# Kernel tuning notes

Hardware: AMD Instinct MI355X
Metric: run time of the kernel (lower is better)

The kernel has to match this reference:

```python
import math
import jax, jax.numpy as jnp
from jax import lax
import numpy as np

# Dimensions (see shape_source)
B, CIN, COUT, H, W = 4, 256, 256, 128, 128
STYLE_DIM = 512
K = 3            # modulated-conv kernel
N_TAPS = 12      # FIR taps
UP, DOWN = 2, 2
UP_PAD, DOWN_PAD = 6, 5   # symmetric pads for up/down FIR stages
SLOPE = 0.2
CLAMP = 256.0
EPS = 1e-8


def _kaiser_lowpass(n_taps, cutoff, band_half, sr):
    # exact port of kaiser_window/lowpass_filter (1-D, use_jinc=False)
    df = 2.0 * band_half / (sr / 2.0)
    atten = 2.285 * (n_taps - 1) * math.pi * df + 7.95
    if atten > 50:
        beta = 0.1102 * (atten - 8.7)
    elif atten >= 21:
        beta = 0.5842 * (atten - 21) ** 0.4 + 0.07886 * (atten - 21)
    else:
        beta = 0.0
    ind = np.arange(n_taps) - (n_taps - 1) / 2.0
    window = np.i0(beta * np.sqrt(1 - (2 * ind / (n_taps - 1)) ** 2)) / np.i0(beta)
    f = 2 * cutoff / sr * np.sinc(2 * cutoff / sr * ind) * window
    return f.astype(np.float32)


def setup_inputs() -> dict:
    key = jax.random.key(0)
    k0, k1, k2, k3 = jax.random.split(key, 4)
    inputs = {
        "input": jax.random.normal(k0, (B, CIN, H, W), jnp.float32),
        "style": jax.random.normal(k1, (B, STYLE_DIM), jnp.float32),
        "weight": jax.random.normal(k2, (COUT, CIN, K, K), jnp.float32),
        "mod_weight": jax.random.normal(k3, (CIN, STYLE_DIM), jnp.float32),
        "mod_bias": jnp.ones((CIN,), jnp.float32),     # EqualLinear bias_init=1
        "bias": jnp.zeros((COUT,), jnp.float32),
        "up_filter": jnp.asarray(_kaiser_lowpass(N_TAPS, cutoff=H / 2, band_half=H / 2, sr=2 * H)),
        "down_filter": jnp.asarray(_kaiser_lowpass(N_TAPS, cutoff=H / 2, band_half=H / 2, sr=2 * H)),
    }
    return inputs


def _upfirdn2d_sep(x, f, up, down, pad):
    # separable depthwise FIR with zero-stuffed upsampling (lhs_dilation)
    c = x.shape[1]
    t = f.shape[0]
    fv = jnp.tile(f.reshape(1, 1, t, 1), (c, 1, 1, 1))
    x = lax.conv_general_dilated(x, fv, window_strides=(down, 1),
                                 padding=((pad, pad), (0, 0)), lhs_dilation=(up, 1),
                                 feature_group_count=c,
                                 dimension_numbers=("NCHW", "OIHW", "NCHW"))
    fh = jnp.tile(f.reshape(1, 1, 1, t), (c, 1, 1, 1))
    x = lax.conv_general_dilated(x, fh, window_strides=(1, down),
                                 padding=((0, 0), (pad, pad)), lhs_dilation=(1, up),
                                 feature_group_count=c,
                                 dimension_numbers=("NCHW", "OIHW", "NCHW"))
    return x


def reference(input, style, weight, mod_weight, mod_bias, bias, up_filter, down_filter):
    b, cin, h, w = input.shape
    # EqualLinear modulation: scale = 1/sqrt(style_dim), lr_mul=1, bias_init=1
    s = style @ mod_weight.T * (1.0 / math.sqrt(STYLE_DIM)) + mod_bias          # [B,Cin]
    # ModulatedConv2d (eval mode: input_gain = rsqrt(ema_var=1) = 1)
    w_mod = weight[None] * s[:, None, :, None, None]                            # [B,Cout,Cin,k,k]
    demod = lax.rsqrt(jnp.sum(w_mod * w_mod, axis=(2, 3, 4)) + EPS)             # [B,Cout]
    w_mod = (w_mod * demod[:, :, None, None, None]).reshape(b * COUT, cin, K, K)
    x = input.reshape(1, b * cin, h, w)
    out = lax.conv_general_dilated(x, w_mod, (1, 1),
                                   ((K - 1, K - 1), (K - 1, K - 1)),
                                   feature_group_count=b,
                                   dimension_numbers=("NCHW", "OIHW", "NCHW"))
    out = out.reshape(b, COUT, out.shape[2], out.shape[3])                      # [B,Cout,130,130]
    # filtered_lrelu: bias -> FIR up x2 (gain up^2 = up per separable pass)
    out = out + bias[None, :, None, None]
    out = _upfirdn2d_sep(out, up_filter * UP, UP, 1, UP_PAD)                    # [B,Cout,260,260]
    out = jnp.where(out >= 0, out, SLOPE * out) * math.sqrt(2.0)                # lrelu, gain sqrt(2)
    out = jnp.clip(out, -CLAMP, CLAMP)
    out = _upfirdn2d_sep(out, down_filter, 1, DOWN, DOWN_PAD)                   # [B,Cout,130,130]
    return out
```

## Files before the change

### kernel.cpp

```cpp
#include <hip/hip_runtime.h>
#include <hip/hip_bf16.h>
#include <math.h>

#define B_    4
#define CIN_  256
#define COUT_ 256
#define H_    128
#define W_    128
#define HW_   16384
#define SD_   512
#define HO_   130
#define HU_   260
#define NT_   12

typedef unsigned short ushort_t;
typedef __attribute__((ext_vector_type(8))) short short8;
typedef __attribute__((ext_vector_type(4))) float f32x4;

__device__ inline ushort_t f2bf_(float v) {
  union { float f; unsigned u; } x; x.f = v;
  unsigned r = x.u + 0x7fffu + ((x.u >> 16) & 1u);
  return (ushort_t)(r >> 16);
}
__device__ inline void gll16(const ushort_t* g, ushort_t* l) {
  __builtin_amdgcn_global_load_lds(
      (const __attribute__((address_space(1))) unsigned int*)g,
      (__attribute__((address_space(3))) unsigned int*)l, 16, 0, 0);
}

__global__ __launch_bounds__(256) void k_mod(const float* __restrict__ style,
                                             const float* __restrict__ mw,
                                             const float* __restrict__ mb,
                                             float* __restrict__ s) {
  int wid  = (blockIdx.x * blockDim.x + threadIdx.x) >> 6;
  int lane = threadIdx.x & 63;
  int b = wid >> 8, ci = wid & 255;
  const float* st = style + b * SD_;
  const float* w  = mw + ci * SD_;
  float acc = 0.f;
  for (int k = lane; k < SD_; k += 64) acc += st[k] * w[k];
  for (int off = 32; off; off >>= 1) acc += __shfl_down(acc, off);
  if (lane == 0) s[wid] = acc * 0.044194173824159216f + mb[ci];
}

__global__ __launch_bounds__(256) void k_demod(const float* __restrict__ weight,
                                               const float* __restrict__ s,
                                               float* __restrict__ demod) {
  int wid  = (blockIdx.x * blockDim.x + threadIdx.x) >> 6;
  int lane = threadIdx.x & 63;
  int b = wid >> 8, co = wid & 255;
  const float* wrow = weight + co * CIN_ * 9;
  const float* sb   = s + b * CIN_;
  float acc = 0.f;
  for (int e = lane; e < CIN_ * 9; e += 64) {
    float p = wrow[e] * sb[e / 9];
    acc += p * p;
  }
  for (int off = 32; off; off >>= 1) acc += __shfl_down(acc, off);
  if (lane == 0) demod[wid] = rsqrtf(acc + 1e-8f);
}

__global__ __launch_bounds__(256) void k_prep_w(const float* __restrict__ W,
                                                ushort_t* __restrict__ Wth) {
  int idx = blockIdx.x * 256 + threadIdx.x;
  if (idx >= 589824) return;
  int j  = idx & 7;
  int co = (idx >> 3) & 127;
  int kc = (idx >> 10) & 3;
  int kb = (idx >> 12) & 7;
  int cb = (idx >> 15) & 1;
  int t  = idx >> 16;
  int ci  = kb * 32 + kc * 8 + j;
  int cog = cb * 128 + co;
  Wth[idx] = f2bf_(W[(cog * CIN_ + ci) * 9 + t]);
}

__global__ __launch_bounds__(256) void k_prep_x(const float* __restrict__ input,
                                                const float* __restrict__ s,
                                                ushort_t* __restrict__ Xt,
                                                float* __restrict__ zp) {
  int b = blockIdx.z, cb = blockIdx.y, px0 = blockIdx.x * 64;
  int tid = threadIdx.x;
  __shared__ float T[64 * 131];
  __shared__ float sSh[128];
  if (tid < 128) sSh[tid] = s[b * 256 + cb * 128 + tid];
  if (blockIdx.x == 0 && blockIdx.y == 0 && blockIdx.z == 0 && tid < 4)
    zp[tid] = 0.f;
  __syncthreads();
  const float* inb = input + (size_t)(b * 256 + cb * 128) * HW_ + px0;
#pragma unroll
  for (int r2 = 0; r2 < 32; ++r2) {
    int idx = r2 * 256 + tid;
    int ci = idx >> 6, p = idx & 63;
    T[p * 131 + ci] = inb[(size_t)ci * HW_ + p] * sSh[ci];
  }
  __syncthreads();
  ushort_t* xb = Xt + (size_t)b * HW_ * 256 + cb * 128;
#pragma unroll
  for (int r2 = 0; r2 < 16; ++r2) {
    int u = r2 * 256 + tid;
    int cp = u & 63, p = u >> 6;
    float v0 = T[p * 131 + 2 * cp], v1 = T[p * 131 + 2 * cp + 1];
    unsigned pk = (unsigned)f2bf_(v0) | ((unsigned)f2bf_(v1) << 16);
    *(unsigned*)(xb + ((size_t)(px0 + p)) * 256 + cp * 2) = pk;
  }
}

#define XCELLS 864
#define XROUNDS 4
#define XBUFU  1024

__global__ __launch_bounds__(256, 3) void k_conv_mfma(
    const ushort_t* __restrict__ Xt, const ushort_t* __restrict__ Wth,
    const float* __restrict__ demod, const float* __restrict__ bias,
    const ushort_t* __restrict__ zpg, float* __restrict__ out1) {
  const int tid = threadIdx.x;
  const int b = blockIdx.z >> 1, cb = blockIdx.z & 1;
  const int y0 = blockIdx.y * 10, x0 = blockIdx.x * 16;
  const int lane = tid & 63, lr = lane & 15, kcc = lane >> 4;
  const int w = tid >> 6;

  __shared__ __align__(16) ushort_t XL[2][XBUFU * 8];

  f32x4 acc[2][10];
#pragma unroll
  for (int i = 0; i < 2; ++i)
#pragma unroll
    for (int jj = 0; jj < 10; ++jj) acc[i][jj] = (f32x4)0.f;

  const ushort_t* gsrc[XROUNDS];
  bool okr[XROUNDS];
#pragma unroll
  for (int r = 0; r < XROUNDS; ++r) {
    int u = r * 256 + tid;
    const ushort_t* p = zpg;
    bool ok = false;
    if (u < XCELLS) {
      int kc = u / 216, cell = u - kc * 216;
      int hy = cell / 18, hx = cell - hy * 18;
      int iy = y0 + hy - 2, ix = x0 + hx - 2;
      if ((unsigned)iy < 128u && (unsigned)ix < 128u) {
        p = Xt + (((size_t)b * HW_ + iy * W_ + ix) << 8) + kc * 8;
        ok = true;
      }
    }
    gsrc[r] = p; okr[r] = ok;
  }

  auto stage = [&](int kb, int bufsel) {
    ushort_t* lb = &XL[bufsel][(size_t)tid * 8];
#pragma unroll
    for (int r = 0; r < XROUNDS; ++r) {
      const ushort_t* g = okr[r] ? gsrc[r] + kb * 32 : zpg;
      gll16(g, lb + r * 2048);
    }
  };

  stage(0, 0);
  __syncthreads();

  for (int kb = 0; kb < 8; ++kb) {
    const ushort_t* Xc = &XL[kb & 1][0];
    const int wbo = cb * 32768 + kb * 4096 + kcc * 1024 + (w * 32 + lr) * 8;
#pragma unroll
    for (int kx = 0; kx < 3; ++kx) {
      short8 ah[3][2];
#pragma unroll
      for (int ky = 0; ky < 3; ++ky) {
        const ushort_t* wh = Wth + wbo + (ky * 3 + kx) * 65536;
        ah[ky][0] = *(const short8*)wh;
        ah[ky][1] = *(const short8*)(wh + 128);
      }
      if (kx == 0) {
        __builtin_amdgcn_sched_barrier(0);
        if (kb < 7) stage(kb + 1, (kb & 1) ^ 1);
      }
#pragma unroll
      for (int r = 0; r < 12; ++r) {
        const int c16 = (kcc * 216 + r * 18 + lr + kx) * 8;
        short8 bh = *(const short8*)&Xc[c16];
#pragma unroll
        for (int ky = 0; ky < 3; ++ky) {
          const int bn = r - ky;
          if (bn >= 0 && bn < 10) {
            acc[0][bn] = __builtin_amdgcn_mfma_f32_16x16x32_bf16(ah[ky][0], bh, acc[0][bn], 0, 0, 0);
            acc[1][bn] = __builtin_amdgcn_mfma_f32_16x16x32_bf16(ah[ky][1], bh, acc[1][bn], 0, 0, 0);
          }
        }
      }
    }
    if (kb < 7) __syncthreads();
  }

#pragma unroll
  for (int am = 0; am < 2; ++am) {
#pragma unroll
    for (int r = 0; r < 4; ++r) {
      int cog = cb * 128 + w * 32 + am * 16 + kcc * 4 + r;
      float dm = demod[b * 256 + cog];
      float bv = bias[cog];
      int ox = x0 + lr;
      if (ox < HO_) {
#pragma unroll
        for (int bn = 0; bn < 10; ++bn) {
          int oy = y0 + bn;
          out1[((b * 256 + cog) * HO_ + oy) * HO_ + ox] = acc[am][bn][r] * dm + bv;
        }
      }
    }
  }
}

#define I1S 132
#define I2S 260

__global__ __launch_bounds__(256) void k_fir(const float* __restrict__ src,
                                             const float* __restrict__ upf,
                                             const float* __restrict__ dnf,
                                             float* __restrict__ dst) {
  const int plane = blockIdx.y;
  const int y0 = blockIdx.x * 8;
  const int tid = threadIdx.x;

  __shared__ __align__(16) float I1D[26 * I1S];
  __shared__ __align__(16) float B2[26 * I2S];

  float* SD = B2;
  float* I2 = B2;
  float* I1 = I1D;
  float* D  = I1D;

  float fe[6], fo[6], fdt[12];
#pragma unroll
  for (int j = 0; j < 6; ++j) { fe[j] = upf[2 * j] * 2.f; fo[j] = upf[2 * j + 1] * 2.f; }
#pragma unroll
  for (int t = 0; t < NT_; ++t) fdt[t] = dnf[t];
  const float kPos = 1.41421356237309515f, kNeg = 0.28284271247461903f;

  const float* sp = src + (size_t)plane * (HO_ * HO_);
#pragma unroll
  for (int k = 0; k < 3; ++k) {
    int idx = tid + k * 256;
    if (idx < 594) {
      int r = idx / 33, q = idx - 33 * r;
      int gy = y0 - 5 + r;
      int cbase = 4 * q;
      float4 v = make_float4(0.f, 0.f, 0.f, 0.f);
      if ((unsigned)gy < (unsigned)HO_) {
        const float* rp = sp + gy * HO_ + cbase;
        v.x = rp[0];
        v.y = (cbase + 1 < HO_) ? rp[1] : 0.f;
        v.z = (cbase + 2 < HO_) ? rp[2] : 0.f;
        v.w = (cbase + 3 < HO_) ? rp[3] : 0.f;
      }
      *(float4*)&SD[r * 132 + cbase] = v;
    }
  }
  __syncthreads();

  {
    int c = tid & 127, uh = tid >> 7;
    float wv[6];
    if (uh == 0) {
#pragma unroll
      for (int j = 0; j < 6; ++j) wv[j] = SD[j * 132 + c];
#pragma unroll
      for (int lr = 0; lr < 7; ++lr) {
        float a = fo[0]*wv[0] + fo[1]*wv[1] + fo[2]*wv[2] + fo[3]*wv[3] + fo[4]*wv[4] + fo[5]*wv[5];
        int ugl = 2 * y0 - 5 + 2 * lr;
        I1[(2 * lr) * I1S + c] = ((unsigned)ugl < (unsigned)HU_) ? a : 0.f;
        if (lr < 6) {
#pragma unroll
          for (int j = 0; j < 5; ++j) wv[j] = wv[j + 1];
          wv[5] = SD[(lr + 6) * 132 + c];
        }
      }
#pragma unroll
      for (int j = 0; j < 6; ++j) wv[j] = SD[j * 132 + c];
#pragma unroll
      for (int lr = 0; lr < 6; ++lr) {
        float a = fe[0]*wv[0] + fe[1]*wv[1] + fe[2]*wv[2] + fe[3]*wv[3] + fe[4]*wv[4] + fe[5]*wv[5];
        int ugl = 2 * y0 - 4 + 2 * lr;
        I1[(2 * lr + 1) * I1S + c] = ((unsigned)ugl < (unsigned)HU_) ? a : 0.f;
        if (lr < 5) {
#pragma unroll
          for (int j = 0; j < 5; ++j) wv[j] = wv[j + 1];
          wv[5] = SD[(lr + 6) * 132 + c];
        }
      }
    } else {
#pragma unroll
      for (int j = 0; j < 6; ++j) wv[j] = SD[(6 + j) * 132 + c];
#pragma unroll
      for (int lr = 6; lr < 13; ++lr) {
        float a = fe[0]*wv[0] + fe[1]*wv[1] + fe[2]*wv[2] + fe[3]*wv[3] + fe[4]*wv[4] + fe[5]*wv[5];
        int ugl = 2 * y0 - 4 + 2 * lr;
        I1[(2 * lr + 1) * I1S + c] = ((unsigned)ugl < (unsigned)HU_) ? a : 0.f;
        if (lr < 12) {
#pragma unroll
          for (int j = 0; j < 5; ++j) wv[j] = wv[j + 1];
          wv[5] = SD[(lr + 6) * 132 + c];
        }
      }
#pragma unroll
      for (int j = 0; j < 6; ++j) wv[j] = SD[(7 + j) * 132 + c];
#pragma unroll
      for (int lr = 7; lr < 13; ++lr) {
        float a = fo[0]*wv[0] + fo[1]*wv[1] + fo[2]*wv[2] + fo[3]*wv[3] + fo[4]*wv[4] + fo[5]*wv[5];
        int ugl = 2 * y0 - 5 + 2 * lr;
        I1[(2 * lr) * I1S + c] = ((unsigned)ugl < (unsigned)HU_) ? a : 0.f;
        if (lr < 12) {
#pragma unroll
          for (int j = 0; j < 5; ++j) wv[j] = wv[j + 1];
          wv[5] = SD[(lr + 6) * 132 + c];
        }
      }
    }
    if (tid >= 200 && tid < 252) {
      int t2 = tid - 200;
      int c2 = 128 + (t2 & 1), u2 = t2 >> 1;
      float a = 0.f;
      if ((u2 & 1) == 0) {
        int lr = u2 >> 1;
#pragma unroll
        for (int j = 0; j < 6; ++j) a += fo[j] * SD[(lr + j) * 132 + c2];
      } else {
        int lr = (u2 - 1) >> 1;
#pragma unroll
        for (int j = 0; j < 6; ++j) a += fe[j] * SD[(lr + j) * 132 + c2];
      }
      int ugl = 2 * y0 - 5 + u2;
      I1[u2 * I1S + c2] = ((unsigned)ugl < (unsigned)HU_) ? a : 0.f;
    }
    if (tid < 52) {
      int r = tid >> 1, col = 130 + (tid & 1);
      I1[r * I1S + col] = 0.f;
    }
  }
  __syncthreads();

  for (int idx = tid; idx < 26 * 33; idx += 256) {
    int s = idx / 26, u = idx - 26 * s;
    const float* I1r = &I1[u * I1S];
    if (s < 32) {
      float w12[12];
      if (s == 0) {
        float4 qb = *(const float4*)&I1r[0];
        float4 qc = *(const float4*)&I1r[4];
        w12[0] = 0.f; w12[1] = 0.f; w12[2] = 0.f; w12[3] = 0.f;
        w12[4] = qb.x; w12[5] = qb.y; w12[6] = qb.z; w12[7] = qb.w;
        w12[8] = qc.x; w12[9] = qc.y; w12[10] = qc.z; w12[11] = qc.w;
      } else {
        int c0 = 4 * s;
        float4 qa = *(const float4*)&I1r[c0 - 4];
        float4 qb = *(const float4*)&I1r[c0];
        float4 qc = *(const float4*)&I1r[c0 + 4];
        w12[0] = qa.x; w12[1] = qa.y; w12[2] = qa.z; w12[3] = qa.w;
        w12[4] = qb.x; w12[5] = qb.y; w12[6] = qb.z; w12[7] = qb.w;
        w12[8] = qc.x; w12[9] = qc.y; w12[10] = qc.z; w12[11] = qc.w;
      }
      float o[8];
#pragma unroll
      for (int e = 0; e < 4; ++e) {
        o[2*e]   = fe[0]*w12[e+1] + fe[1]*w12[e+2] + fe[2]*w12[e+3] + fe[3]*w12[e+4] + fe[4]*w12[e+5] + fe[5]*w12[e+6];
        o[2*e+1] = fo[0]*w12[e+2] + fo[1]*w12[e+3] + fo[2]*w12[e+4] + fo[3]*w12[e+5] + fo[4]*w12[e+6] + fo[5]*w12[e+7];
      }
#pragma unroll
      for (int e = 0; e < 8; ++e) {
        float a = o[e];
        float m = (a >= 0.f) ? kPos : kNeg;
        a *= m;
        o[e] = fminf(fmaxf(a, -256.f), 256.f);
      }
      *(float4*)&I2[u * I2S + 8 * s]     = make_float4(o[0], o[1], o[2], o[3]);
      *(float4*)&I2[u * I2S + 8 * s + 4] = make_float4(o[4], o[5], o[6], o[7]);
    } else {
      float4 qa = *(const float4*)&I1r[124];
      float4 qb = *(const float4*)&I1r[128];
      float w8[8] = {qa.x, qa.y, qa.z, qa.w, qb.x, qb.y, qb.z, qb.w};
      float q[4];
      q[0] = fe[0]*w8[1] + fe[1]*w8[2] + fe[2]*w8[3] + fe[3]*w8[4] + fe[4]*w8[5] + fe[5]*w8[6];
      q[1] = fo[0]*w8[2] + fo[1]*w8[3] + fo[2]*w8[4] + fo[3]*w8[5] + fo[4]*w8[6] + fo[5]*w8[7];
      q[2] = fe[0]*w8[2] + fe[1]*w8[3] + fe[2]*w8[4] + fe[3]*w8[5] + fe[4]*w8[6] + fe[5]*w8[7];
      q[3] = fo[0]*w8[3] + fo[1]*w8[4] + fo[2]*w8[5] + fo[3]*w8[6] + fo[4]*w8[7];
      float q2[4];
#pragma unroll
      for (int e = 0; e < 4; ++e) {
        float a = q[e];
        float m = (a >= 0.f) ? kPos : kNeg;
        a *= m;
        q2[e] = fminf(fmaxf(a, -256.f), 256.f);
      }
      *(float4*)&I2[u * I2S + 256] = make_float4(q2[0], q2[1], q2[2], q2[3]);
    }
  }
  __syncthreads();

  {
    if (tid < 96) {
      int r = tid / 12, j = tid - 12 * r;
      int col = (j < 5) ? j : (260 + j);
      D[r * 272 + col] = 0.f;
    }
    auto p3col = [&](int v) {
      float wn[12];
#pragma unroll
      for (int t = 0; t < 12; ++t) wn[t] = I2[t * I2S + v];
#pragma unroll
      for (int y = 0; y < 8; ++y) {
        float a = 0.f;
#pragma unroll
        for (int t = 0; t < 12; ++t) a += fdt[t] * wn[t];
        D[y * 272 + v + 5] = a;
        if (y < 7) {
#pragma unroll
          for (int t = 0; t < 10; ++t) wn[t] = wn[t + 2];
          wn[10] = I2[(2 * y + 12) * I2S + v];
          wn[11] = I2[(2 * y + 13) * I2S + v];
        }
      }
    };
    p3col(tid);
    if (tid < 4) p3col(256 + tid);
  }
  __syncthreads();

  if (tid < 208) {
    int row = tid / 26, s4 = tid - 26 * row;
    int gy = y0 + row;
    if (gy < HO_) {
      float wn[20];
#pragma unroll
      for (int k = 0; k < 10; ++k) {
        float2 t2 = *(const float2*)&D[row * 272 + 10 * s4 + 2 * k];
        wn[2 * k] = t2.x;
        wn[2 * k + 1] = t2.y;
      }
      float* dp = dst + (size_t)plane * (HO_ * HO_) + gy * HO_ + 5 * s4;
#pragma unroll
      for (int q = 0; q < 5; ++q) {
        float a = 0.f;
#pragma unroll
        for (int t = 0; t < 12; ++t) a += fdt[t] * wn[2 * q + t];
        dp[q] = a;
      }
    }
  }
}

extern "C" void kernel_launch(void* const* d_in, const int* in_sizes, int n_in,
                              void* d_out, int out_size, void* d_ws, size_t ws_size,
                              hipStream_t stream) {
  (void)in_sizes; (void)n_in; (void)out_size; (void)ws_size;
  const float* input  = (const float*)d_in[0];
  const float* style  = (const float*)d_in[1];
  const float* weight = (const float*)d_in[2];
  const float* mw     = (const float*)d_in[3];
  const float* mb     = (const float*)d_in[4];
  const float* bias   = (const float*)d_in[5];
  const float* upf    = (const float*)d_in[6];
  const float* dnf    = (const float*)d_in[7];
  float* out = (float*)d_out;

  float* out1   = (float*)d_ws;
  float* s      = out1 + (size_t)B_ * COUT_ * HO_ * HO_;
  float* demod  = s + B_ * CIN_;
  ushort_t* Wth = (ushort_t*)(demod + B_ * COUT_);
  float*    zp  = (float*)(Wth + 589824);
  ushort_t* Xt  = (ushort_t*)(zp + 4);

  k_mod   <<<256, 256, 0, stream>>>(style, mw, mb, s);
  k_prep_x<<<dim3(256, 2, B_), 256, 0, stream>>>(input, s, Xt, zp);
  k_demod <<<256, 256, 0, stream>>>(weight, s, demod);
  k_prep_w<<<2304, 256, 0, stream>>>(weight, Wth);
  k_conv_mfma<<<dim3(9, 13, 8), 256, 0, stream>>>(Xt, Wth, demod, bias,
                                                  (const ushort_t*)zp, out1);
  k_fir   <<<dim3(17, 1024), 256, 0, stream>>>(out1, upf, dnf, out);
}
```

Before: 234.1 us.

## Process two channel planes per FIR block using packed float2 math

The FIR kernel now processes two channel planes per block. Shared-memory buffers hold interleaved float2 pairs and all filter arithmetic runs on 2-wide vectors, which can map to packed FMA instructions. The grid is halved to 512 plane-pairs. This amortizes index arithmetic and filter setup per element and improves ILP, at the cost of doubled LDS use per block (~80KB), which likely reduces occupancy.

```diff
diff --git a/kernel.cpp b/kernel.cpp
--- a/kernel.cpp
+++ b/kernel.cpp
@@ -16,6 +16,7 @@
 typedef unsigned short ushort_t;
 typedef __attribute__((ext_vector_type(8))) short short8;
 typedef __attribute__((ext_vector_type(4))) float f32x4;
+typedef __attribute__((ext_vector_type(2))) float f32x2;
 
 __device__ inline ushort_t f2bf_(float v) {
   union { float f; unsigned u; } x; x.f = v;
@@ -218,17 +219,17 @@
                                              const float* __restrict__ upf,
                                              const float* __restrict__ dnf,
                                              float* __restrict__ dst) {
-  const int plane = blockIdx.y;
+  const int pp = blockIdx.y;
   const int y0 = blockIdx.x * 8;
   const int tid = threadIdx.x;
 
-  __shared__ __align__(16) float I1D[26 * I1S];
-  __shared__ __align__(16) float B2[26 * I2S];
-
-  float* SD = B2;
-  float* I2 = B2;
-  float* I1 = I1D;
-  float* D  = I1D;
+  __shared__ __align__(16) f32x2 I1D[26 * I1S];
+  __shared__ __align__(16) f32x2 B2[26 * I2S];
+
+  f32x2* SD = B2;
+  f32x2* I2 = B2;
+  f32x2* I1 = I1D;
+  f32x2* D  = I1D;
 
   float fe[6], fo[6], fdt[12];
 #pragma unroll
@@ -237,7 +238,17 @@
   for (int t = 0; t < NT_; ++t) fdt[t] = dnf[t];
   const float kPos = 1.41421356237309515f, kNeg = 0.28284271247461903f;
 
-  const float* sp = src + (size_t)plane * (HO_ * HO_);
+  auto lrc = [&](f32x2 a) {
+    float x = a.x, y = a.y;
+    x *= (x >= 0.f) ? kPos : kNeg;
+    y *= (y >= 0.f) ? kPos : kNeg;
+    x = fminf(fmaxf(x, -256.f), 256.f);
+    y = fminf(fmaxf(y, -256.f), 256.f);
+    return (f32x2){x, y};
+  };
+
+  const float* sp0 = src + (size_t)(2 * pp) * (HO_ * HO_);
+  const float* sp1 = sp0 + HO_ * HO_;
 #pragma unroll
   for (int k = 0; k < 3; ++k) {
     int idx = tid + k * 256;
@@ -245,30 +256,36 @@
       int r = idx / 33, q = idx - 33 * r;
       int gy = y0 - 5 + r;
       int cbase = 4 * q;
-      float4 v = make_float4(0.f, 0.f, 0.f, 0.f);
+      float4 a = make_float4(0.f, 0.f, 0.f, 0.f);
+      float4 b = a;
       if ((unsigned)gy < (unsigned)HO_) {
-        const float* rp = sp + gy * HO_ + cbase;
-        v.x = rp[0];
-        v.y = (cbase + 1 < HO_) ? rp[1] : 0.f;
-        v.z = (cbase + 2 < HO_) ? rp[2] : 0.f;
-        v.w = (cbase + 3 < HO_) ? rp[3] : 0.f;
-      }
-      *(float4*)&SD[r * 132 + cbase] = v;
+        const float* r0 = sp0 + gy * HO_ + cbase;
+        const float* r1 = sp1 + gy * HO_ + cbase;
+        a.x = r0[0];                       b.x = r1[0];
+        if (cbase + 1 < HO_) { a.y = r0[1]; b.y = r1[1]; }
+        if (cbase + 2 < HO_) { a.z = r0[2]; b.z = r1[2]; }
+        if (cbase + 3 < HO_) { a.w = r0[3]; b.w = r1[3]; }
+      }
+      f32x2* d = &SD[r * 132 + cbase];
+      d[0] = (f32x2){a.x, b.x};
+      d[1] = (f32x2){a.y, b.y};
+      d[2] = (f32x2){a.z, b.z};
+      d[3] = (f32x2){a.w, b.w};
     }
   }
   __syncthreads();
 
   {
     int c = tid & 127, uh = tid >> 7;
-    float wv[6];
+    f32x2 wv[6];
     if (uh == 0) {
 #pragma unroll
       for (int j = 0; j < 6; ++j) wv[j] = SD[j * 132 + c];
 #pragma unroll
       for (int lr = 0; lr < 7; ++lr) {
-        float a = fo[0]*wv[0] + fo[1]*wv[1] + fo[2]*wv[2] + fo[3]*wv[3] + fo[4]*wv[4] + fo[5]*wv[5];
+        f32x2 a = fo[0]*wv[0] + fo[1]*wv[1] + fo[2]*wv[2] + fo[3]*wv[3] + fo[4]*wv[4] + fo[5]*wv[5];
         int ugl = 2 * y0 - 5 + 2 * lr;
-        I1[(2 * lr) * I1S + c] = ((unsigned)ugl < (unsigned)HU_) ? a : 0.f;
+        I1[(2 * lr) * I1S + c] = ((unsigned)ugl < (unsigned)HU_) ? a : (f32x2)0.f;
         if (lr < 6) {
 #pragma unroll
           for (int j = 0; j < 5; ++j) wv[j] = wv[j + 1];
@@ -279,9 +296,9 @@
       for (int j = 0; j < 6; ++j) wv[j] = SD[j * 132 + c];
 #pragma unroll
       for (int lr = 0; lr < 6; ++lr) {
-        float a = fe[0]*wv[0] + fe[1]*wv[1] + fe[2]*wv[2] + fe[3]*wv[3] + fe[4]*wv[4] + fe[5]*wv[5];
+        f32x2 a = fe[0]*wv[0] + fe[1]*wv[1] + fe[2]*wv[2] + fe[3]*wv[3] + fe[4]*wv[4] + fe[5]*wv[5];
         int ugl = 2 * y0 - 4 + 2 * lr;
-        I1[(2 * lr + 1) * I1S + c] = ((unsigned)ugl < (unsigned)HU_) ? a : 0.f;
+        I1[(2 * lr + 1) * I1S + c] = ((unsigned)ugl < (unsigned)HU_) ? a : (f32x2)0.f;
         if (lr < 5) {
 #pragma unroll
           for (int j = 0; j < 5; ++j) wv[j] = wv[j + 1];
@@ -293,9 +310,9 @@
       for (int j = 0; j < 6; ++j) wv[j] = SD[(6 + j) * 132 + c];
 #pragma unroll
       for (int lr = 6; lr < 13; ++lr) {
-        float a = fe[0]*wv[0] + fe[1]*wv[1] + fe[2]*wv[2] + fe[3]*wv[3] + fe[4]*wv[4] + fe[5]*wv[5];
+        f32x2 a = fe[0]*wv[0] + fe[1]*wv[1] + fe[2]*wv[2] + fe[3]*wv[3] + fe[4]*wv[4] + fe[5]*wv[5];
         int ugl = 2 * y0 - 4 + 2 * lr;
-        I1[(2 * lr + 1) * I1S + c] = ((unsigned)ugl < (unsigned)HU_) ? a : 0.f;
+        I1[(2 * lr + 1) * I1S + c] = ((unsigned)ugl < (unsigned)HU_) ? a : (f32x2)0.f;
         if (lr < 12) {
 #pragma unroll
           for (int j = 0; j < 5; ++j) wv[j] = wv[j + 1];
@@ -306,9 +323,9 @@
       for (int j = 0; j < 6; ++j) wv[j] = SD[(7 + j) * 132 + c];
 #pragma unroll
       for (int lr = 7; lr < 13; ++lr) {
-        float a = fo[0]*wv[0] + fo[1]*wv[1] + fo[2]*wv[2] + fo[3]*wv[3] + fo[4]*wv[4] + fo[5]*wv[5];
+        f32x2 a = fo[0]*wv[0] + fo[1]*wv[1] + fo[2]*wv[2] + fo[3]*wv[3] + fo[4]*wv[4] + fo[5]*wv[5];
         int ugl = 2 * y0 - 5 + 2 * lr;
-        I1[(2 * lr) * I1S + c] = ((unsigned)ugl < (unsigned)HU_) ? a : 0.f;
+        I1[(2 * lr) * I1S + c] = ((unsigned)ugl < (unsigned)HU_) ? a : (f32x2)0.f;
         if (lr < 12) {
 #pragma unroll
           for (int j = 0; j < 5; ++j) wv[j] = wv[j + 1];
@@ -319,7 +336,7 @@
     if (tid >= 200 && tid < 252) {
       int t2 = tid - 200;
       int c2 = 128 + (t2 & 1), u2 = t2 >> 1;
-      float a = 0.f;
+      f32x2 a = (f32x2)0.f;
       if ((u2 & 1) == 0) {
         int lr = u2 >> 1;
 #pragma unroll
@@ -330,68 +347,64 @@
         for (int j = 0; j < 6; ++j) a += fe[j] * SD[(lr + j) * 132 + c2];
       }
       int ugl = 2 * y0 - 5 + u2;
-      I1[u2 * I1S + c2] = ((unsigned)ugl < (unsigned)HU_) ? a : 0.f;
+      I1[u2 * I1S + c2] = ((unsigned)ugl < (unsigned)HU_) ? a : (f32x2)0.f;
     }
     if (tid < 52) {
       int r = tid >> 1, col = 130 + (tid & 1);
-      I1[r * I1S + col] = 0.f;
-    }
-  }
-  __syncthreads();
-
+      I1[r * I1S + col] = (f32x2)0.f;
+    }
+  }
+  __syncthreads();
+
+  auto ld2 = [&](const f32x2* p, f32x2& a, f32x2& b) {
+    f32x4 t = *(const f32x4*)p;
+    a = (f32x2){t.x, t.y};
+    b = (f32x2){t.z, t.w};
+  };
   for (int idx = tid; idx < 26 * 33; idx += 256) {
     int s = idx / 26, u = idx - 26 * s;
-    const float* I1r = &I1[u * I1S];
+    const f32x2* I1r = &I1[u * I1S];
     if (s < 32) {
-      float w12[12];
+      f32x2 w12[12];
       if (s == 0) {
-        float4 qb = *(const float4*)&I1r[0];
-        float4 qc = *(const float4*)&I1r[4];
-        w12[0] = 0.f; w12[1] = 0.f; w12[2] = 0.f; w12[3] = 0.f;
-        w12[4] = qb.x; w12[5] = qb.y; w12[6] = qb.z; w12[7] = qb.w;
-        w12[8] = qc.x; w12[9] = qc.y; w12[10] = qc.z; w12[11] = qc.w;
+        w12[0] = w12[1] = w12[2] = w12[3] = (f32x2)0.f;
+        ld2(&I1r[0], w12[4], w12[5]);
+        ld2(&I1r[2], w12[6], w12[7]);
+        ld2(&I1r[4], w12[8], w12[9]);
+        ld2(&I1r[6], w12[10], w12[11]);
       } else {
         int c0 = 4 * s;
-        float4 qa = *(const float4*)&I1r[c0 - 4];
-        float4 qb = *(const float4*)&I1r[c0];
-        float4 qc = *(const float4*)&I1r[c0 + 4];
-        w12[0] = qa.x; w12[1] = qa.y; w12[2] = qa.z; w12[3] = qa.w;
-        w12[4] = qb.x; w12[5] = qb.y; w12[6] = qb.z; w12[7] = qb.w;
-        w12[8] = qc.x; w12[9] = qc.y; w12[10] = qc.z; w12[11] = qc.w;
-      }
-      float o[8];
+#pragma unroll
+        for (int h = 0; h < 6; ++h)
+          ld2(&I1r[c0 - 4 + 2 * h], w12[2 * h], w12[2 * h + 1]);
+      }
+      f32x2 o[8];
 #pragma unroll
       for (int e = 0; e < 4; ++e) {
         o[2*e]   = fe[0]*w12[e+1] + fe[1]*w12[e+2] + fe[2]*w12[e+3] + fe[3]*w12[e+4] + fe[4]*w12[e+5] + fe[5]*w12[e+6];
         o[2*e+1] = fo[0]*w12[e+2] + fo[1]*w12[e+3] + fo[2]*w12[e+4] + fo[3]*w12[e+5] + fo[4]*w12[e+6] + fo[5]*w12[e+7];
       }
 #pragma unroll
-      for (int e = 0; e < 8; ++e) {
-        float a = o[e];
-        float m = (a >= 0.f) ? kPos : kNeg;
-        a *= m;
-        o[e] = fminf(fmaxf(a, -256.f), 256.f);
-      }
-      *(float4*)&I2[u * I2S + 8 * s]     = make_float4(o[0], o[1], o[2], o[3]);
-      *(float4*)&I2[u * I2S + 8 * s + 4] = make_float4(o[4], o[5], o[6], o[7]);
+      for (int e = 0; e < 8; ++e) o[e] = lrc(o[e]);
+#pragma unroll
+      for (int h = 0; h < 4; ++h)
+        *(f32x4*)&I2[u * I2S + 8 * s + 2 * h] =
+            (f32x4){o[2*h].x, o[2*h].y, o[2*h+1].x, o[2*h+1].y};
     } else {
-      float4 qa = *(const float4*)&I1r[124];
-      float4 qb = *(const float4*)&I1r[128];
-      float w8[8] = {qa.x, qa.y, qa.z, qa.w, qb.x, qb.y, qb.z, qb.w};
-      float q[4];
+      f32x2 w8[8];
+      ld2(&I1r[124], w8[0], w8[1]);
+      ld2(&I1r[126], w8[2], w8[3]);
+      ld2(&I1r[128], w8[4], w8[5]);
+      ld2(&I1r[130], w8[6], w8[7]);
+      f32x2 q[4];
       q[0] = fe[0]*w8[1] + fe[1]*w8[2] + fe[2]*w8[3] + fe[3]*w8[4] + fe[4]*w8[5] + fe[5]*w8[6];
       q[1] = fo[0]*w8[2] + fo[1]*w8[3] + fo[2]*w8[4] + fo[3]*w8[5] + fo[4]*w8[6] + fo[5]*w8[7];
       q[2] = fe[0]*w8[2] + fe[1]*w8[3] + fe[2]*w8[4] + fe[3]*w8[5] + fe[4]*w8[6] + fe[5]*w8[7];
       q[3] = fo[0]*w8[3] + fo[1]*w8[4] + fo[2]*w8[5] + fo[3]*w8[6] + fo[4]*w8[7];
-      float q2[4];
-#pragma unroll
-      for (int e = 0; e < 4; ++e) {
-        float a = q[e];
-        float m = (a >= 0.f) ? kPos : kNeg;
-        a *= m;
-        q2[e] = fminf(fmaxf(a, -256.f), 256.f);
-      }
-      *(float4*)&I2[u * I2S + 256] = make_float4(q2[0], q2[1], q2[2], q2[3]);
+#pragma unroll
+      for (int e = 0; e < 4; ++e) q[e] = lrc(q[e]);
+      *(f32x4*)&I2[u * I2S + 256] = (f32x4){q[0].x, q[0].y, q[1].x, q[1].y};
+      *(f32x4*)&I2[u * I2S + 258] = (f32x4){q[2].x, q[2].y, q[3].x, q[3].y};
     }
   }
   __syncthreads();
@@ -400,15 +413,15 @@
     if (tid < 96) {
       int r = tid / 12, j = tid - 12 * r;
       int col = (j < 5) ? j : (260 + j);
-      D[r * 272 + col] = 0.f;
+      D[r * 272 + col] = (f32x2)0.f;
     }
     auto p3col = [&](int v) {
-      float wn[12];
+      f32x2 wn[12];
 #pragma unroll
       for (int t = 0; t < 12; ++t) wn[t] = I2[t * I2S + v];
 #pragma unroll
       for (int y = 0; y < 8; ++y) {
-        float a = 0.f;
+        f32x2 a = (f32x2)0.f;
 #pragma unroll
         for (int t = 0; t < 12; ++t) a += fdt[t] * wn[t];
         D[y * 272 + v + 5] = a;
@@ -429,20 +442,19 @@
     int row = tid / 26, s4 = tid - 26 * row;
     int gy = y0 + row;
     if (gy < HO_) {
-      float wn[20];
-#pragma unroll
-      for (int k = 0; k < 10; ++k) {
-        float2 t2 = *(const float2*)&D[row * 272 + 10 * s4 + 2 * k];
-        wn[2 * k] = t2.x;
-        wn[2 * k + 1] = t2.y;
-      }
-      float* dp = dst + (size_t)plane * (HO_ * HO_) + gy * HO_ + 5 * s4;
+      f32x2 wn[20];
+#pragma unroll
+      for (int k = 0; k < 10; ++k)
+        ld2(&D[row * 272 + 10 * s4 + 2 * k], wn[2 * k], wn[2 * k + 1]);
+      float* d0 = dst + (size_t)(2 * pp) * (HO_ * HO_) + gy * HO_ + 5 * s4;
+      float* d1 = d0 + HO_ * HO_;
 #pragma unroll
       for (int q = 0; q < 5; ++q) {
-        float a = 0.f;
+        f32x2 a = (f32x2)0.f;
 #pragma unroll
         for (int t = 0; t < 12; ++t) a += fdt[t] * wn[2 * q + t];
-        dp[q] = a;
+        d0[q] = a.x;
+        d1[q] = a.y;
       }
     }
   }
@@ -475,5 +487,5 @@
   k_prep_w<<<2304, 256, 0, stream>>>(weight, Wth);
   k_conv_mfma<<<dim3(9, 13, 8), 256, 0, stream>>>(Xt, Wth, demod, bias,
                                                   (const ushort_t*)zp, out1);
-  k_fir   <<<dim3(17, 1024), 256, 0, stream>>>(out1, upf, dnf, out);
-}
+  k_fir   <<<dim3(17, 512), 256, 0, stream>>>(out1, upf, dnf, out);
+}
```

New measurement: 240.6 us. 2.8% more time.
